# Performance work log

Hardware: AMD Instinct MI355X
Metric: run time of the kernel (lower is better)

Reference implementation:

```python
import jax, jax.numpy as jnp
import numpy as np

LMAX = 4
NC = (LMAX + 1) ** 2  # 25 spherical-harmonic coefficients
L_IDX = np.repeat(np.arange(LMAX + 1), 2 * np.arange(LMAX + 1) + 1)  # degree of each coeff


def so3_linear(x, w, b):
    # x: [N, NC, Cin]; w: [LMAX+1, Cin, Cout]; bias only on l=0 coefficient
    wexp = w[jnp.asarray(L_IDX)]  # [NC, Cin, Cout]
    out = jnp.einsum("nic,icd->nid", x, wexp)
    return out.at[:, 0, :].add(b)


def setup_inputs() -> dict:
    key = jax.random.key(0)
    ks = jax.random.split(key, 12)
    N, C = 2048, 128
    R = 18
    s = 0.05
    return {
        "x": jax.random.normal(ks[0], (N, NC, C), jnp.float32),
        "w1": jax.random.normal(ks[1], (LMAX + 1, C, C), jnp.float32) * s,
        "b1": jax.random.normal(ks[2], (C,), jnp.float32) * s,
        "ws": jax.random.normal(ks[3], (C, C), jnp.float32) * s,
        "bs": jax.random.normal(ks[4], (C,), jnp.float32) * s,
        "wg1": jax.random.normal(ks[5], (C, C), jnp.float32) * s,
        "wg2": jax.random.normal(ks[6], (C, C), jnp.float32) * s,
        "wg3": jax.random.normal(ks[7], (C, C), jnp.float32) * s,
        "w2": jax.random.normal(ks[8], (LMAX + 1, C, C), jnp.float32) * s,
        "b2": jax.random.normal(ks[9], (C,), jnp.float32) * s,
        "to_grid_mat": jax.random.normal(ks[10], (R, R, NC), jnp.float32) * 0.2,
        "from_grid_mat": jax.random.normal(ks[11], (R, R, NC), jnp.float32) * 0.2,
    }


def reference(x, w1, b1, ws, bs, wg1, wg2, wg3, w2, b2, to_grid_mat, from_grid_mat):
    # separable-S2 gating scalars from the l=0 component of the input
    gating = jax.nn.silu(x[:, 0:1, :] @ ws + bs)  # [N, 1, C]
    # SO3 linear 1 (per-degree weights, bias on l=0)
    h = so3_linear(x, w1, b1)  # [N, NC, H]
    # to grid: [res_beta, res_alpha, NC] x [N, NC, H] -> [N, rb, ra, H]
    g = jnp.einsum("bai,nic->nbac", to_grid_mat, h)
    # grid MLP: Linear->SiLU->Linear->SiLU->Linear (no biases)
    g = jax.nn.silu(g @ wg1)
    g = jax.nn.silu(g @ wg2)
    g = g @ wg3
    # from grid back to SH coefficients
    h = jnp.einsum("bai,nbac->nic", from_grid_mat, g)  # [N, NC, H]
    # replace l=0 coefficient with gating scalars
    h = jnp.concatenate([gating, h[:, 1:, :]], axis=1)
    # SO3 linear 2
    return so3_linear(h, w2, b2)
```

## Files before the change

kernel.cpp:

```cpp
#include <hip/hip_runtime.h>
#include <hip/hip_bf16.h>

typedef unsigned short u16;
typedef unsigned int u32;
typedef __attribute__((ext_vector_type(8))) short short8;
typedef __attribute__((ext_vector_type(8))) __bf16 bf16x8;
typedef __attribute__((ext_vector_type(4))) float f32x4;

__device__ __forceinline__ float bf2f(u16 u) {
    union { float f; unsigned int i; } v; v.i = ((unsigned int)u) << 16; return v.f;
}
__device__ __forceinline__ u16 f2bf(float f) {
    u32 b = __builtin_bit_cast(u32, f);
    b += 0x7FFFu + ((b >> 16) & 1u);
    return (u16)(b >> 16);
}
__device__ __forceinline__ u32 f2bf2(float f0, float f1) {
    u32 b0 = __builtin_bit_cast(u32, f0);
    u32 b1 = __builtin_bit_cast(u32, f1);
    b0 += 0x7FFFu + ((b0 >> 16) & 1u);
    b1 += 0x7FFFu + ((b1 >> 16) & 1u);
    return (b0 >> 16) | (b1 & 0xFFFF0000u);
}
__device__ __forceinline__ float silu_f(float v) {
    return v * __builtin_amdgcn_rcpf(1.0f + __expf(-v));
}
__device__ __forceinline__ unsigned swz(unsigned row, unsigned colbyte) {
    return row * 256u + (colbyte ^ ((row & 7u) << 4));
}
__device__ __forceinline__ f32x4 MFMA(short8 a, short8 b, f32x4 c) {
    return __builtin_amdgcn_mfma_f32_16x16x32_bf16(
        __builtin_bit_cast(bf16x8, a), __builtin_bit_cast(bf16x8, b), c, 0, 0, 0);
}

#define SW1 40
#define SGT 72

#define OFF_W1T 0
#define OFF_W2T 81920
#define OFF_WGT 163840
#define OFF_TGP 212992
#define OFF_FGT 225280
#define OFF_WSB 237568
#define OFF_B1B 253952
#define OFF_BSB 254080
#define OFF_B2B 254208
#define PREP_TOTAL 254336
#define OFF_FLAG 254336

__global__ void detect_kernel(const void* __restrict__ x, u32* __restrict__ flagp) {
    int tid = threadIdx.x;
    const u16* p = (const u16*)x;
    int cnt = 0;
    #pragma unroll
    for (int j = 0; j < 8; ++j) {
        float v = fabsf(bf2f(p[2 * (tid * 8 + j)]));
        if (v >= 1e-4f && v <= 100.0f) ++cnt;
    }
    #pragma unroll
    for (int d = 32; d; d >>= 1) cnt += __shfl_down(cnt, d);
    if (tid == 0) *flagp = (cnt >= 256) ? 1u : 0u;
}

__global__ void prep_kernel(const void* __restrict__ w1, const void* __restrict__ wg1,
                            const void* __restrict__ wg2, const void* __restrict__ wg3,
                            const void* __restrict__ w2, const void* __restrict__ tg,
                            const void* __restrict__ fg, const void* __restrict__ wsm,
                            const void* __restrict__ b1, const void* __restrict__ bs,
                            const void* __restrict__ b2,
                            u16* __restrict__ wsp, const u32* __restrict__ flagp) {
    const int flag = (int)*flagp;
    int idx = blockIdx.x * 256 + threadIdx.x;
    if (idx >= PREP_TOTAL) return;
    auto ld = [&](const void* p, int s) -> u16 {
        return flag ? ((const u16*)p)[s] : f2bf(((const float*)p)[s]);
    };
    if (idx < OFF_W2T) {
        int l = idx >> 14, c = (idx >> 7) & 127, k = idx & 127;
        wsp[idx] = ld(w1, (l << 14) + (k << 7) + c);
    } else if (idx < OFF_WGT) {
        int j = idx - OFF_W2T;
        int l = j >> 14, c = (j >> 7) & 127, k = j & 127;
        wsp[idx] = ld(w2, (l << 14) + (k << 7) + c);
    } else if (idx < OFF_TGP) {
        int j = idx - OFF_WGT;
        int m = j >> 14, c = (j >> 7) & 127, k = j & 127;
        const void* w = (m == 0) ? wg1 : (m == 1) ? wg2 : wg3;
        wsp[idx] = ld(w, (k << 7) + c);
    } else if (idx < OFF_FGT) {
        int j = idx - OFF_TGP;
        int r = j >> 5, i = j & 31;
        wsp[idx] = (r < 324 && i < 25) ? ld(tg, r * 25 + i) : (u16)0;
    } else if (idx < OFF_WSB) {
        int j = idx - OFF_FGT;
        int i = j / 384, r = j % 384;
        wsp[idx] = (i < 25 && r < 324) ? ld(fg, r * 25 + i) : (u16)0;
    } else if (idx < OFF_B1B) {
        int j = idx - OFF_WSB;
        wsp[idx] = ld(wsm, ((j & 127) << 7) + (j >> 7));
    } else if (idx < OFF_BSB) {
        wsp[idx] = ld(b1, idx - OFF_B1B);
    } else if (idx < OFF_B2B) {
        wsp[idx] = ld(bs, idx - OFF_BSB);
    } else {
        wsp[idx] = ld(b2, idx - OFF_B2B);
    }
}

__global__ __launch_bounds__(256, 3) void ffn_kernel(
    const void* __restrict__ xin, const u16* __restrict__ wsp,
    void* __restrict__ outp) {
    const u16* w1T  = wsp + OFF_W1T;
    const u16* w2T  = wsp + OFF_W2T;
    const u16* wg1T = wsp + OFF_WGT;
    const u16* wg2T = wsp + OFF_WGT + 16384;
    const u16* wg3T = wsp + OFF_WGT + 32768;
    const u16* tgp  = wsp + OFF_TGP;
    const u16* fgT  = wsp + OFF_FGT;
    const u16* wsT  = wsp + OFF_WSB;
    const u16* b1b  = wsp + OFF_B1B;
    const u16* bsb  = wsp + OFF_BSB;
    const u16* b2b  = wsp + OFF_B2B;
    const int flag = (int)*(const u32*)(wsp + OFF_FLAG);

    __shared__ u16 ldsA[64 * 128];
    __shared__ u16 hw1T[128 * SW1];
    __shared__ u16 gTl[128 * SGT];

    const int tid = threadIdx.x;
    const int w = tid >> 6;
    const int lane = tid & 63;
    const int lq = lane >> 4;
    const int lr = lane & 15;
    const int n = blockIdx.x;

    char* gA_b = reinterpret_cast<char*>(ldsA);
    char* xs_b = gA_b;
    char* hs_b = gA_b + 32 * 256;
    const short8 zero8 = {0, 0, 0, 0, 0, 0, 0, 0};
    const int cc0 = (w * 2) * 16 + lr, cc1 = (w * 2 + 1) * 16 + lr;

    {
        #pragma unroll
        for (int v = 0; v < 4; ++v) {
            int idx = tid + v * 256;
            int row = idx >> 5, c4 = idx & 31;
            ushort4 val = make_ushort4(0, 0, 0, 0);
            if (row < 25) {
                if (flag) {
                    val = *reinterpret_cast<const ushort4*>(
                        (const u16*)xin + (size_t)n * 3200 + row * 128 + c4 * 4);
                } else {
                    float4 f = *reinterpret_cast<const float4*>(
                        (const float*)xin + (size_t)n * 3200 + row * 128 + c4 * 4);
                    val.x = f2bf(f.x); val.y = f2bf(f.y);
                    val.z = f2bf(f.z); val.w = f2bf(f.w);
                }
            }
            *reinterpret_cast<ushort4*>(xs_b + swz(row, c4 * 8)) = val;
        }
        for (int i = tid; i < 448; i += 256)
            ((u32*)(hs_b + 25 * 256))[i] = 0;
    }
    __syncthreads();

    f32x4 gate_v[2];
    {
        #pragma unroll
        for (int nn = 0; nn < 2; ++nn) {
            int cc = nn ? cc1 : cc0;
            f32x4 acc = {0.f, 0.f, 0.f, 0.f};
            #pragma unroll
            for (int ks = 0; ks < 4; ++ks) {
                short8 a = *reinterpret_cast<const short8*>(
                    wsT + cc * 128 + ks * 32 + lq * 8);
                short8 b = zero8;
                if (lr == 0)
                    b = *reinterpret_cast<const short8*>(
                        xs_b + swz(0, ks * 64 + lq * 16));
                acc = MFMA(a, b, acc);
            }
            #pragma unroll
            for (int r = 0; r < 4; ++r) {
                int c = (w * 2 + nn) * 16 + lq * 4 + r;
                gate_v[nn][r] = silu_f(acc[r] + bf2f(bsb[c]));
            }
        }
        const int m0[5] = {0, 1, 4, 9, 16};
        const int ml[5] = {1, 3, 5, 7, 9};
        #pragma unroll
        for (int l = 0; l < 5; ++l) {
            bool valid = lr < ml[l];
            #pragma unroll
            for (int nn = 0; nn < 2; ++nn) {
                int c = (w * 2 + nn) * 16 + lr;
                f32x4 acc = {0.f, 0.f, 0.f, 0.f};
                #pragma unroll
                for (int ks = 0; ks < 4; ++ks) {
                    short8 av = *reinterpret_cast<const short8*>(
                        xs_b + swz(m0[l] + lr, (ks * 32 + lq * 8) * 2));
                    short8 a = valid ? av : zero8;
                    short8 b = *reinterpret_cast<const short8*>(
                        w1T + (l * 128 + c) * 128 + ks * 32 + lq * 8);
                    acc = MFMA(a, b, acc);
                }
                #pragma unroll
                for (int r = 0; r < 4; ++r) {
                    int mm = lq * 4 + r;
                    if (mm < ml[l]) {
                        int i = m0[l] + mm;
                        float v2 = acc[r] + ((i == 0) ? bf2f(b1b[c]) : 0.f);
                        *reinterpret_cast<u16*>(hs_b + swz(i, c * 2)) = f2bf(v2);
                    }
                }
            }
        }
    }
    __syncthreads();

    {
        #pragma unroll
        for (int mt = 0; mt < 2; ++mt) {
            #pragma unroll
            for (int nn = 0; nn < 2; ++nn) {
                int cc = nn ? cc1 : cc0;
                f32x4 acc = {0.f, 0.f, 0.f, 0.f};
                #pragma unroll
                for (int ks = 0; ks < 4; ++ks) {
                    short8 a = *reinterpret_cast<const short8*>(
                        hs_b + swz(mt * 16 + lr, (ks * 32 + lq * 8) * 2));
                    short8 b = *reinterpret_cast<const short8*>(
                        wg1T + cc * 128 + ks * 32 + lq * 8);
                    acc = MFMA(a, b, acc);
                }
                uint2 pk;
                pk.x = f2bf2(acc[0], acc[1]);
                pk.y = f2bf2(acc[2], acc[3]);
                *reinterpret_cast<uint2*>(&hw1T[cc * SW1 + mt * 16 + lq * 4]) = pk;
            }
        }
    }
    __syncthreads();

    short8 bh[2];
    short8 bfr[2][4];
    #pragma unroll
    for (int nn = 0; nn < 2; ++nn) {
        int cc = nn ? cc1 : cc0;
        bh[nn] = *reinterpret_cast<const short8*>(&hw1T[cc * SW1 + lq * 8]);
        #pragma unroll
        for (int ks = 0; ks < 4; ++ks)
            bfr[nn][ks] = *reinterpret_cast<const short8*>(
                wg2T + cc * 128 + ks * 32 + lq * 8);
    }

    f32x4 facc[2][2];
    #pragma unroll
    for (int i = 0; i < 2; ++i)
        #pragma unroll
        for (int j = 0; j < 2; ++j) facc[i][j] = f32x4{0.f, 0.f, 0.f, 0.f};

    for (int ch = 0; ch < 6; ++ch) {
        #pragma unroll
        for (int mt = 0; mt < 4; ++mt) {
            short8 tgf = *reinterpret_cast<const short8*>(
                tgp + (ch * 64 + mt * 16 + lr) * 32 + lq * 8);
            #pragma unroll
            for (int nn = 0; nn < 2; ++nn) {
                f32x4 acc = MFMA(bh[nn], tgf, f32x4{0.f, 0.f, 0.f, 0.f});
                uint2 pk;
                pk.x = f2bf2(silu_f(acc[0]), silu_f(acc[1]));
                pk.y = f2bf2(silu_f(acc[2]), silu_f(acc[3]));
                *reinterpret_cast<uint2*>(
                    gA_b + swz(mt * 16 + lr, (w * 2 + nn) * 32 + lq * 8)) = pk;
            }
        }
        __syncthreads();

        #pragma unroll
        for (int mt = 0; mt < 4; ++mt) {
            f32x4 a0 = {0.f, 0.f, 0.f, 0.f}, a1v = {0.f, 0.f, 0.f, 0.f};
            #pragma unroll
            for (int ks = 0; ks < 4; ++ks) {
                short8 af = *reinterpret_cast<const short8*>(
                    gA_b + swz(mt * 16 + lr, ks * 64 + lq * 16));
                a0 = MFMA(af, bfr[0][ks], a0);
                a1v = MFMA(af, bfr[1][ks], a1v);
            }
            uint2 p0, p1;
            p0.x = f2bf2(silu_f(a0[0]), silu_f(a0[1]));
            p0.y = f2bf2(silu_f(a0[2]), silu_f(a0[3]));
            p1.x = f2bf2(silu_f(a1v[0]), silu_f(a1v[1]));
            p1.y = f2bf2(silu_f(a1v[2]), silu_f(a1v[3]));
            *reinterpret_cast<uint2*>(&gTl[cc0 * SGT + mt * 16 + lq * 4]) = p0;
            *reinterpret_cast<uint2*>(&gTl[cc1 * SGT + mt * 16 + lq * 4]) = p1;
        }
        __syncthreads();

        #pragma unroll
        for (int it = 0; it < 2; ++it) {
            #pragma unroll
            for (int ks = 0; ks < 2; ++ks) {
                short8 bf_ = *reinterpret_cast<const short8*>(
                    fgT + (it * 16 + lr) * 384 + ch * 64 + ks * 32 + lq * 8);
                #pragma unroll
                for (int nn = 0; nn < 2; ++nn) {
                    short8 ag = *reinterpret_cast<const short8*>(
                        &gTl[(nn ? cc1 : cc0) * SGT + ks * 32 + lq * 8]);
                    facc[nn][it] = MFMA(ag, bf_, facc[nn][it]);
                }
            }
        }
    }

    #pragma unroll
    for (int nn = 0; nn < 2; ++nn)
        #pragma unroll
        for (int it = 0; it < 2; ++it) {
            uint2 pk;
            pk.x = f2bf2(facc[nn][it][0], facc[nn][it][1]);
            pk.y = f2bf2(facc[nn][it][2], facc[nn][it][3]);
            *reinterpret_cast<uint2*>(
                xs_b + swz(it * 16 + lr, (w * 2 + nn) * 32 + lq * 8)) = pk;
        }
    __syncthreads();

    #pragma unroll
    for (int it = 0; it < 2; ++it) {
        #pragma unroll
        for (int nn = 0; nn < 2; ++nn) {
            int cc = nn ? cc1 : cc0;
            f32x4 acc = {0.f, 0.f, 0.f, 0.f};
            #pragma unroll
            for (int ks = 0; ks < 4; ++ks) {
                short8 a = *reinterpret_cast<const short8*>(
                    wg3T + cc * 128 + ks * 32 + lq * 8);
                short8 b = *reinterpret_cast<const short8*>(
                    xs_b + swz(it * 16 + lr, ks * 64 + lq * 16));
                acc = MFMA(a, b, acc);
            }
            if (it == 0 && lr == 0) acc = gate_v[nn];
            uint2 pk;
            pk.x = f2bf2(acc[0], acc[1]);
            pk.y = f2bf2(acc[2], acc[3]);
            *reinterpret_cast<uint2*>(
                hs_b + swz(it * 16 + lr, (w * 2 + nn) * 32 + lq * 8)) = pk;
        }
    }
    __syncthreads();

    {
        const int m0[5] = {0, 1, 4, 9, 16};
        const int ml[5] = {1, 3, 5, 7, 9};
        #pragma unroll
        for (int l = 0; l < 5; ++l) {
            bool valid = lr < ml[l];
            #pragma unroll
            for (int nn = 0; nn < 2; ++nn) {
                int c = (w * 2 + nn) * 16 + lr;
                f32x4 acc = {0.f, 0.f, 0.f, 0.f};
                #pragma unroll
                for (int ks = 0; ks < 4; ++ks) {
                    short8 av = *reinterpret_cast<const short8*>(
                        hs_b + swz(m0[l] + lr, (ks * 32 + lq * 8) * 2));
                    short8 a = valid ? av : zero8;
                    short8 b = *reinterpret_cast<const short8*>(
                        w2T + (l * 128 + c) * 128 + ks * 32 + lq * 8);
                    acc = MFMA(a, b, acc);
                }
                #pragma unroll
                for (int r = 0; r < 4; ++r) {
                    int mm = lq * 4 + r;
                    if (mm < ml[l]) {
                        int i = m0[l] + mm;
                        float v2 = acc[r] + ((i == 0) ? bf2f(b2b[c]) : 0.f);
                        size_t o = (size_t)n * 3200 + i * 128 + c;
                        if (flag) ((u16*)outp)[o] = f2bf(v2);
                        else      ((float*)outp)[o] = v2;
                    }
                }
            }
        }
    }
}

extern "C" void kernel_launch(void* const* d_in, const int* in_sizes, int n_in,
                              void* d_out, int out_size, void* d_ws, size_t ws_size,
                              hipStream_t stream) {
    const void* x   = d_in[0];
    const void* w1  = d_in[1];
    const void* b1  = d_in[2];
    const void* wsm = d_in[3];
    const void* bs  = d_in[4];
    const void* wg1 = d_in[5];
    const void* wg2 = d_in[6];
    const void* wg3 = d_in[7];
    const void* w2  = d_in[8];
    const void* b2  = d_in[9];
    const void* tg  = d_in[10];
    const void* fg  = d_in[11];
    u16* wsp = (u16*)d_ws;
    u32* flagp = (u32*)(wsp + OFF_FLAG);

    detect_kernel<<<1, 64, 0, stream>>>(x, flagp);
    prep_kernel<<<(PREP_TOTAL + 255) / 256, 256, 0, stream>>>(
        w1, wg1, wg2, wg3, w2, tg, fg, wsm, b1, bs, b2, wsp, flagp);
    ffn_kernel<<<2048, 256, 0, stream>>>(x, wsp, d_out);
}
```

Baseline: 268.4 us.

## Software-pipeline the grid MLP loop with double-buffered LDS and fewer barriers

Splits the 384 grid points into 12 chunks of 32 instead of 6 chunks of 64. The first grid projection, the second MLP layer and the from-grid accumulation now run as a skewed three-stage pipeline over two LDS buffers each, with one barrier per iteration instead of two. The aim is to cut synchronisation stalls and overlap MFMA work from different stages. It uses slightly more LDS for the doubled gTl buffer and issues smaller MFMA batches per stage.

```diff
diff --git a/kernel.cpp b/kernel.cpp
--- a/kernel.cpp
+++ b/kernel.cpp
@@ -34,7 +34,7 @@
 }
 
 #define SW1 40
-#define SGT 72
+#define SGT 40
 
 #define OFF_W1T 0
 #define OFF_W2T 81920
@@ -125,7 +125,7 @@
 
     __shared__ u16 ldsA[64 * 128];
     __shared__ u16 hw1T[128 * SW1];
-    __shared__ u16 gTl[128 * SGT];
+    __shared__ u16 gTl[2][128 * SGT];
 
     const int tid = threadIdx.x;
     const int w = tid >> 6;
@@ -260,11 +260,12 @@
         #pragma unroll
         for (int j = 0; j < 2; ++j) facc[i][j] = f32x4{0.f, 0.f, 0.f, 0.f};
 
-    for (int ch = 0; ch < 6; ++ch) {
-        #pragma unroll
-        for (int mt = 0; mt < 4; ++mt) {
+    auto phase_a = [&](int ch) {
+        char* dst = gA_b + (ch & 1) * 8192;
+        #pragma unroll
+        for (int mt = 0; mt < 2; ++mt) {
             short8 tgf = *reinterpret_cast<const short8*>(
-                tgp + (ch * 64 + mt * 16 + lr) * 32 + lq * 8);
+                tgp + (ch * 32 + mt * 16 + lr) * 32 + lq * 8);
             #pragma unroll
             for (int nn = 0; nn < 2; ++nn) {
                 f32x4 acc = MFMA(bh[nn], tgf, f32x4{0.f, 0.f, 0.f, 0.f});
@@ -272,18 +273,20 @@
                 pk.x = f2bf2(silu_f(acc[0]), silu_f(acc[1]));
                 pk.y = f2bf2(silu_f(acc[2]), silu_f(acc[3]));
                 *reinterpret_cast<uint2*>(
-                    gA_b + swz(mt * 16 + lr, (w * 2 + nn) * 32 + lq * 8)) = pk;
-            }
-        }
-        __syncthreads();
-
-        #pragma unroll
-        for (int mt = 0; mt < 4; ++mt) {
+                    dst + swz(mt * 16 + lr, (w * 2 + nn) * 32 + lq * 8)) = pk;
+            }
+        }
+    };
+    auto phase_b = [&](int ch) {
+        const char* src = gA_b + (ch & 1) * 8192;
+        u16* gdst = &gTl[ch & 1][0];
+        #pragma unroll
+        for (int mt = 0; mt < 2; ++mt) {
             f32x4 a0 = {0.f, 0.f, 0.f, 0.f}, a1v = {0.f, 0.f, 0.f, 0.f};
             #pragma unroll
             for (int ks = 0; ks < 4; ++ks) {
                 short8 af = *reinterpret_cast<const short8*>(
-                    gA_b + swz(mt * 16 + lr, ks * 64 + lq * 16));
+                    src + swz(mt * 16 + lr, ks * 64 + lq * 16));
                 a0 = MFMA(af, bfr[0][ks], a0);
                 a1v = MFMA(af, bfr[1][ks], a1v);
             }
@@ -292,26 +295,41 @@
             p0.y = f2bf2(silu_f(a0[2]), silu_f(a0[3]));
             p1.x = f2bf2(silu_f(a1v[0]), silu_f(a1v[1]));
             p1.y = f2bf2(silu_f(a1v[2]), silu_f(a1v[3]));
-            *reinterpret_cast<uint2*>(&gTl[cc0 * SGT + mt * 16 + lq * 4]) = p0;
-            *reinterpret_cast<uint2*>(&gTl[cc1 * SGT + mt * 16 + lq * 4]) = p1;
-        }
+            *reinterpret_cast<uint2*>(&gdst[cc0 * SGT + mt * 16 + lq * 4]) = p0;
+            *reinterpret_cast<uint2*>(&gdst[cc1 * SGT + mt * 16 + lq * 4]) = p1;
+        }
+    };
+    auto phase_e = [&](int ch) {
+        const u16* gsrc = &gTl[ch & 1][0];
+        #pragma unroll
+        for (int it = 0; it < 2; ++it) {
+            short8 bf_ = *reinterpret_cast<const short8*>(
+                fgT + (it * 16 + lr) * 384 + ch * 32 + lq * 8);
+            #pragma unroll
+            for (int nn = 0; nn < 2; ++nn) {
+                short8 ag = *reinterpret_cast<const short8*>(
+                    &gsrc[(nn ? cc1 : cc0) * SGT + lq * 8]);
+                facc[nn][it] = MFMA(ag, bf_, facc[nn][it]);
+            }
+        }
+    };
+
+    phase_a(0);
+    __syncthreads();
+    phase_b(0);
+    phase_a(1);
+    __syncthreads();
+    #pragma unroll 2
+    for (int k = 0; k <= 9; ++k) {
+        phase_e(k);
+        phase_b(k + 1);
+        phase_a(k + 2);
         __syncthreads();
-
-        #pragma unroll
-        for (int it = 0; it < 2; ++it) {
-            #pragma unroll
-            for (int ks = 0; ks < 2; ++ks) {
-                short8 bf_ = *reinterpret_cast<const short8*>(
-                    fgT + (it * 16 + lr) * 384 + ch * 64 + ks * 32 + lq * 8);
-                #pragma unroll
-                for (int nn = 0; nn < 2; ++nn) {
-                    short8 ag = *reinterpret_cast<const short8*>(
-                        &gTl[(nn ? cc1 : cc0) * SGT + ks * 32 + lq * 8]);
-                    facc[nn][it] = MFMA(ag, bf_, facc[nn][it]);
-                }
-            }
-        }
-    }
+    }
+    phase_e(10);
+    phase_b(11);
+    __syncthreads();
+    phase_e(11);
 
     #pragma unroll
     for (int nn = 0; nn < 2; ++nn)
```

New measurement: 264.1 us. No clear change (-1.6%).
